# Performance work log

Hardware: AMD Instinct MI355X
Metric: run time of the kernel (lower is better)

Reference implementation:

```python
import jax, jax.numpy as jnp
import numpy as np

ALPHA = 32.0
RANK = 16
SCALE = ALPHA / RANK


def setup_inputs() -> dict:
    key = jax.random.key(0)
    k1, k2, k3, k4, k5 = jax.random.split(key, 5)
    B, S, D_IN, D_OUT, N = 4, 2048, 4096, 4096, 8
    x = jax.random.normal(k1, (B, S, D_IN), dtype=jnp.float32)
    routing_w = jax.random.uniform(k2, (B, N), dtype=jnp.float32)
    W_base = jax.random.normal(k3, (D_OUT, D_IN), dtype=jnp.float32) * 0.02
    lora_down = jax.random.normal(k4, (N, RANK, D_IN), dtype=jnp.float32) * 0.02
    lora_up = jax.random.normal(k5, (N, D_OUT, RANK), dtype=jnp.float32) * 0.02
    return {"x": x, "routing_w": routing_w, "W_base": W_base,
            "lora_down": lora_down, "lora_up": lora_up}


def reference(x, routing_w, W_base, lora_down, lora_up):
    # base linear: [B,S,D_in] @ [D_out,D_in]^T -> [B,S,D_out]
    base_out = jnp.einsum('bsi,oi->bso', x, W_base)
    # per-expert LoRA down-proj: [B,S,D_in] x [N,R,D_in] -> [B,N,S,R]
    down = jnp.einsum('bsi,nri->bnsr', x, lora_down)
    # up-proj + scale: [B,N,S,R] x [N,D_out,R] -> [B,N,S,D_out]
    up = jnp.einsum('bnsr,nor->bnso', down, lora_up) * SCALE
    # routing-weighted sum over experts: [B,N] x [B,N,S,D_out] -> [B,S,D_out]
    adapter_out = jnp.einsum('bn,bnso->bso', routing_w, up)
    return base_out + adapter_out
```

## Files before the change

kernel.cpp:

```cpp
#include <hip/hip_runtime.h>
#include <hip/hip_bf16.h>
#include <stdint.h>

#define TOK    8192
#define DIN    4096
#define DOUT   4096
#define NEXP   8
#define RK     16
#define NRANK  128
#define KE     4224
#define SEQB   2048
#define LSCALE 2.0f
#define KSPLIT 4
#define KSLICE (DIN / KSPLIT)

typedef __attribute__((ext_vector_type(8))) short bf8_t;
typedef __attribute__((ext_vector_type(4))) float f4_t;

__device__ __forceinline__ void async_copy16(const void* g, void* l) {
  __builtin_amdgcn_global_load_lds((const __attribute__((address_space(1))) void*)g,
                                   (__attribute__((address_space(3))) void*)l,
                                   16, 0, 0);
}

__device__ __forceinline__ ushort f2bf(float f) {
  __hip_bfloat16 h = __float2bfloat16(f);
  return *reinterpret_cast<ushort*>(&h);
}

#define R0 (TOK * DIN / 8)
#define R1 (DOUT * DIN / 8)
#define R2 (DOUT * NEXP * 2)
#define R3 (NRANK * DIN / 8)
#define RTOT (R0 + R1 + R2 + R3)

__global__ __launch_bounds__(256)
void cvt_all_kernel(const float* __restrict__ x, const float* __restrict__ wb,
                    const float* __restrict__ lu, const float* __restrict__ ld,
                    ushort* __restrict__ Xe, ushort* __restrict__ Wc,
                    ushort* __restrict__ Ldb) {
  int i = blockIdx.x * 256 + threadIdx.x;
  const float* src;
  ushort* dst;
  if (i < R0) {
    int t = i >> 9;
    int c = (i & 511) * 8;
    src = x + (size_t)t * DIN + c;
    dst = Xe + (size_t)t * KE + c;
  } else if (i < R0 + R1) {
    int j = i - R0;
    int t = j >> 9;
    int c = (j & 511) * 8;
    src = wb + (size_t)t * DIN + c;
    dst = Wc + (size_t)t * KE + c;
  } else if (i < R0 + R1 + R2) {
    int j = i - (R0 + R1);
    int o = j >> 4;
    int rem = j & 15;
    int n = rem >> 1;
    int half = rem & 1;
    src = lu + ((size_t)n * DOUT + o) * RK + half * 8;
    dst = Wc + (size_t)o * KE + DIN + n * RK + half * 8;
  } else {
    int j = i - (R0 + R1 + R2);
    src = ld + (size_t)j * 8;
    dst = Ldb + (size_t)j * 8;
  }
  const float4* s = reinterpret_cast<const float4*>(src);
  float4 a = s[0], b = s[1];
  union { ushort u[8]; uint4 v; } o;
  o.u[0]=f2bf(a.x); o.u[1]=f2bf(a.y); o.u[2]=f2bf(a.z); o.u[3]=f2bf(a.w);
  o.u[4]=f2bf(b.x); o.u[5]=f2bf(b.y); o.u[6]=f2bf(b.z); o.u[7]=f2bf(b.w);
  *reinterpret_cast<uint4*>(dst) = o.v;
}

template<int KLEN, int LDB, int MODE>
__global__ __launch_bounds__(256)
void gemm128(const ushort* __restrict__ A,
             const ushort* __restrict__ Bm,
             float* __restrict__ C) {
  __shared__ __align__(16) ushort As[128 * 32];
  __shared__ __align__(16) ushort Bs[128 * 32];

  const int tid  = threadIdx.x;
  const int wave = tid >> 6;
  const int lane = tid & 63;

  int bm, bn;
  if (MODE == 0) {
    int bid = blockIdx.x;
    int xcd = bid & 7;
    int idx = bid >> 3;
    int nt  = xcd * 4 + (idx & 3);
    int mt  = idx >> 2;
    bm = mt * 128;
    bn = nt * 128;
  } else {
    bm = blockIdx.y * 128;
    bn = blockIdx.x * 128;
  }
  const int wm = wave & 1, wn = wave >> 1;

  f4_t acc[4][4];
#pragma unroll
  for (int i = 0; i < 4; i++)
#pragma unroll
    for (int j = 0; j < 4; j++) acc[i][j] = (f4_t){0.f, 0.f, 0.f, 0.f};

  const int f0 = tid * 8;
  const int r0 = f0 >> 5, c0 = f0 & 31;
  const int f1 = (256 + tid) * 8;
  const int r1 = f1 >> 5, c1 = f1 & 31;
  const int l0 = (wave << 6) * 8;
  const int l1 = (256 + (wave << 6)) * 8;

  const ushort* Ar = As + (wm * 64 + (lane & 15)) * 32 + (lane >> 4) * 8;
  const ushort* Br = Bs + (wn * 64 + (lane & 15)) * 32 + (lane >> 4) * 8;

  const int kbase = (MODE == 1) ? blockIdx.z * KSLICE : 0;
  const int kend  = kbase + KLEN;

  for (int k0 = kbase; k0 < kend; k0 += 32) {
    __syncthreads();
    async_copy16(A  + (size_t)(bm + r0) * KE  + k0 + c0, (void*)(As + l0));
    async_copy16(A  + (size_t)(bm + r1) * KE  + k0 + c1, (void*)(As + l1));
    async_copy16(Bm + (size_t)(bn + r0) * LDB + k0 + c0, (void*)(Bs + l0));
    async_copy16(Bm + (size_t)(bn + r1) * LDB + k0 + c1, (void*)(Bs + l1));
    __syncthreads();
    bf8_t av[4], bv[4];
#pragma unroll
    for (int i = 0; i < 4; i++) av[i] = *(const bf8_t*)(Ar + i * 16 * 32);
#pragma unroll
    for (int j = 0; j < 4; j++) bv[j] = *(const bf8_t*)(Br + j * 16 * 32);
#pragma unroll
    for (int i = 0; i < 4; i++)
#pragma unroll
      for (int j = 0; j < 4; j++)
        acc[i][j] = __builtin_amdgcn_mfma_f32_16x16x32_bf16(av[i], bv[j], acc[i][j], 0, 0, 0);
  }

  if (MODE == 0) {
#pragma unroll
    for (int i = 0; i < 4; i++) {
      int row = bm + wm * 64 + i * 16 + (lane >> 4) * 4;
#pragma unroll
      for (int j = 0; j < 4; j++) {
        int col = bn + wn * 64 + j * 16 + (lane & 15);
#pragma unroll
        for (int rr = 0; rr < 4; rr++)
          C[(size_t)(row + rr) * DOUT + col] = acc[i][j][rr];
      }
    }
  } else {
    float* Dz = C + (size_t)blockIdx.z * TOK * NRANK;
#pragma unroll
    for (int i = 0; i < 4; i++) {
      int row = bm + wm * 64 + i * 16 + (lane >> 4) * 4;
#pragma unroll
      for (int j = 0; j < 4; j++) {
        int col = wn * 64 + j * 16 + (lane & 15);
#pragma unroll
        for (int rr = 0; rr < 4; rr++)
          Dz[(size_t)(row + rr) * NRANK + col] = acc[i][j][rr];
      }
    }
  }
}

__global__ void scale_store_kernel(const float* __restrict__ D32,
                                   const float* __restrict__ rw,
                                   ushort* __restrict__ Xe) {
  int i = blockIdx.x * 256 + threadIdx.x;
  int t = i >> 5;
  int g = (i & 31) * 4;
  size_t base = (size_t)t * NRANK + g;
  const size_t ss = (size_t)TOK * NRANK;
  float4 a = *reinterpret_cast<const float4*>(D32 + base);
  float4 b = *reinterpret_cast<const float4*>(D32 + ss + base);
  float4 c = *reinterpret_cast<const float4*>(D32 + 2 * ss + base);
  float4 d = *reinterpret_cast<const float4*>(D32 + 3 * ss + base);
  int n = g >> 4;
  int bb = t / SEQB;
  float s = rw[bb * NEXP + n] * LSCALE;
  union { ushort u[4]; uint2 v; } o;
  o.u[0] = f2bf((a.x + b.x + c.x + d.x) * s);
  o.u[1] = f2bf((a.y + b.y + c.y + d.y) * s);
  o.u[2] = f2bf((a.z + b.z + c.z + d.z) * s);
  o.u[3] = f2bf((a.w + b.w + c.w + d.w) * s);
  *reinterpret_cast<uint2*>(Xe + (size_t)t * KE + DIN + g) = o.v;
}

extern "C" void kernel_launch(void* const* d_in, const int* in_sizes, int n_in,
                              void* d_out, int out_size, void* d_ws, size_t ws_size,
                              hipStream_t stream) {
  const float* x  = (const float*)d_in[0];
  const float* rw = (const float*)d_in[1];
  const float* wb = (const float*)d_in[2];
  const float* ld = (const float*)d_in[3];
  const float* lu = (const float*)d_in[4];
  float* out = (float*)d_out;

  ushort* Xe  = (ushort*)d_ws;
  ushort* Wc  = Xe + (size_t)TOK * KE;
  ushort* Ldb = Wc + (size_t)DOUT * KE;
  float*  D32 = (float*)(Ldb + (size_t)NRANK * DIN);

  cvt_all_kernel<<<RTOT / 256, 256, 0, stream>>>(x, wb, lu, ld, Xe, Wc, Ldb);

  gemm128<KSLICE, DIN, 1><<<dim3(1, TOK / 128, KSPLIT), 256, 0, stream>>>(Xe, Ldb, D32);
  scale_store_kernel<<<TOK * NRANK / 4 / 256, 256, 0, stream>>>(D32, rw, Xe);
  gemm128<KE, KE, 0><<<dim3((TOK / 128) * (DOUT / 128)), 256, 0, stream>>>(Xe, Wc, out);
}
```

Baseline: 673.4 us.

## Use 256x256 double-buffered tiles for main fused GEMM

Splits the templated GEMM into a dedicated down-projection kernel and a new main GEMM. The main GEMM uses 256x256 output tiles with a 128x128 per-wave sub-tile and double-buffered LDS, prefetching the next K-step while the current one computes. The goal is to raise arithmetic intensity and hide global-load latency. The cost is 256 accumulator registers per thread at one block per CU, fewer blocks (512), and a different XCD tile mapping, so spills or low occupancy are possible.

```diff
diff --git a/kernel.cpp b/kernel.cpp
--- a/kernel.cpp
+++ b/kernel.cpp
@@ -74,31 +74,17 @@
   *reinterpret_cast<uint4*>(dst) = o.v;
 }
 
-template<int KLEN, int LDB, int MODE>
 __global__ __launch_bounds__(256)
-void gemm128(const ushort* __restrict__ A,
-             const ushort* __restrict__ Bm,
-             float* __restrict__ C) {
+void gemm_down(const ushort* __restrict__ A,
+               const ushort* __restrict__ Bm,
+               float* __restrict__ C) {
   __shared__ __align__(16) ushort As[128 * 32];
   __shared__ __align__(16) ushort Bs[128 * 32];
 
   const int tid  = threadIdx.x;
   const int wave = tid >> 6;
   const int lane = tid & 63;
-
-  int bm, bn;
-  if (MODE == 0) {
-    int bid = blockIdx.x;
-    int xcd = bid & 7;
-    int idx = bid >> 3;
-    int nt  = xcd * 4 + (idx & 3);
-    int mt  = idx >> 2;
-    bm = mt * 128;
-    bn = nt * 128;
-  } else {
-    bm = blockIdx.y * 128;
-    bn = blockIdx.x * 128;
-  }
+  const int bm = blockIdx.y * 128;
   const int wm = wave & 1, wn = wave >> 1;
 
   f4_t acc[4][4];
@@ -117,15 +103,15 @@
   const ushort* Ar = As + (wm * 64 + (lane & 15)) * 32 + (lane >> 4) * 8;
   const ushort* Br = Bs + (wn * 64 + (lane & 15)) * 32 + (lane >> 4) * 8;
 
-  const int kbase = (MODE == 1) ? blockIdx.z * KSLICE : 0;
-  const int kend  = kbase + KLEN;
+  const int kbase = blockIdx.z * KSLICE;
+  const int kend  = kbase + KSLICE;
 
   for (int k0 = kbase; k0 < kend; k0 += 32) {
     __syncthreads();
     async_copy16(A  + (size_t)(bm + r0) * KE  + k0 + c0, (void*)(As + l0));
     async_copy16(A  + (size_t)(bm + r1) * KE  + k0 + c1, (void*)(As + l1));
-    async_copy16(Bm + (size_t)(bn + r0) * LDB + k0 + c0, (void*)(Bs + l0));
-    async_copy16(Bm + (size_t)(bn + r1) * LDB + k0 + c1, (void*)(Bs + l1));
+    async_copy16(Bm + (size_t)r0 * DIN + k0 + c0, (void*)(Bs + l0));
+    async_copy16(Bm + (size_t)r1 * DIN + k0 + c1, (void*)(Bs + l1));
     __syncthreads();
     bf8_t av[4], bv[4];
 #pragma unroll
@@ -139,30 +125,103 @@
         acc[i][j] = __builtin_amdgcn_mfma_f32_16x16x32_bf16(av[i], bv[j], acc[i][j], 0, 0, 0);
   }
 
-  if (MODE == 0) {
-#pragma unroll
-    for (int i = 0; i < 4; i++) {
-      int row = bm + wm * 64 + i * 16 + (lane >> 4) * 4;
-#pragma unroll
-      for (int j = 0; j < 4; j++) {
-        int col = bn + wn * 64 + j * 16 + (lane & 15);
-#pragma unroll
-        for (int rr = 0; rr < 4; rr++)
-          C[(size_t)(row + rr) * DOUT + col] = acc[i][j][rr];
+  float* Dz = C + (size_t)blockIdx.z * TOK * NRANK;
+#pragma unroll
+  for (int i = 0; i < 4; i++) {
+    int row = bm + wm * 64 + i * 16 + (lane >> 4) * 4;
+#pragma unroll
+    for (int j = 0; j < 4; j++) {
+      int col = wn * 64 + j * 16 + (lane & 15);
+#pragma unroll
+      for (int rr = 0; rr < 4; rr++)
+        Dz[(size_t)(row + rr) * NRANK + col] = acc[i][j][rr];
+    }
+  }
+}
+
+#define NK (KE / 32)
+
+__global__ __launch_bounds__(256, 1)
+void gemm_main(const ushort* __restrict__ A,
+               const ushort* __restrict__ Bm,
+               float* __restrict__ C) {
+  __shared__ __align__(16) ushort As[2][256 * 32];
+  __shared__ __align__(16) ushort Bs[2][256 * 32];
+
+  const int tid  = threadIdx.x;
+  const int wave = tid >> 6;
+  const int lane = tid & 63;
+
+  const int bid = blockIdx.x;
+  const int xcd = bid & 7;
+  const int idx = bid >> 3;
+  const int nt  = xcd * 2 + (idx & 1);
+  const int mt  = idx >> 1;
+  const int bm = mt * 256;
+  const int bn = nt * 256;
+  const int wm = wave & 1, wn = wave >> 1;
+
+  f4_t acc[8][8];
+#pragma unroll
+  for (int i = 0; i < 8; i++)
+#pragma unroll
+    for (int j = 0; j < 8; j++) acc[i][j] = (f4_t){0.f, 0.f, 0.f, 0.f};
+
+  const int srow   = wave * 64 + (lane >> 2);
+  const int schunk = (lane & 3) * 8;
+  const ushort* gA = A  + (size_t)(bm + srow) * KE + schunk;
+  const ushort* gB = Bm + (size_t)(bn + srow) * KE + schunk;
+  const int lbase = wave * 64 * 32;
+
+  const int aoff = (wm * 128 + (lane & 15)) * 32 + (lane >> 4) * 8;
+  const int boff = (wn * 128 + (lane & 15)) * 32 + (lane >> 4) * 8;
+
+  {
+    const ushort* a = gA;
+    const ushort* b = gB;
+#pragma unroll
+    for (int j2 = 0; j2 < 4; j2++) {
+      async_copy16(a + (size_t)j2 * 16 * KE, (void*)(&As[0][lbase + j2 * 16 * 32]));
+      async_copy16(b + (size_t)j2 * 16 * KE, (void*)(&Bs[0][lbase + j2 * 16 * 32]));
+    }
+  }
+
+  for (int k = 0; k < NK; k++) {
+    const int buf = k & 1;
+    __syncthreads();
+    if (k + 1 < NK) {
+      const int nbuf = (k + 1) & 1;
+      const ushort* a = gA + (size_t)(k + 1) * 32;
+      const ushort* b = gB + (size_t)(k + 1) * 32;
+#pragma unroll
+      for (int j2 = 0; j2 < 4; j2++) {
+        async_copy16(a + (size_t)j2 * 16 * KE, (void*)(&As[nbuf][lbase + j2 * 16 * 32]));
+        async_copy16(b + (size_t)j2 * 16 * KE, (void*)(&Bs[nbuf][lbase + j2 * 16 * 32]));
       }
     }
-  } else {
-    float* Dz = C + (size_t)blockIdx.z * TOK * NRANK;
-#pragma unroll
-    for (int i = 0; i < 4; i++) {
-      int row = bm + wm * 64 + i * 16 + (lane >> 4) * 4;
-#pragma unroll
-      for (int j = 0; j < 4; j++) {
-        int col = wn * 64 + j * 16 + (lane & 15);
-#pragma unroll
-        for (int rr = 0; rr < 4; rr++)
-          Dz[(size_t)(row + rr) * NRANK + col] = acc[i][j][rr];
-      }
+    const ushort* Ar = &As[buf][aoff];
+    const ushort* Br = &Bs[buf][boff];
+    bf8_t bv[8];
+#pragma unroll
+    for (int jn = 0; jn < 8; jn++) bv[jn] = *(const bf8_t*)(Br + jn * 16 * 32);
+#pragma unroll
+    for (int i = 0; i < 8; i++) {
+      bf8_t av = *(const bf8_t*)(Ar + i * 16 * 32);
+#pragma unroll
+      for (int jn = 0; jn < 8; jn++)
+        acc[i][jn] = __builtin_amdgcn_mfma_f32_16x16x32_bf16(av, bv[jn], acc[i][jn], 0, 0, 0);
+    }
+  }
+
+#pragma unroll
+  for (int i = 0; i < 8; i++) {
+    int row = bm + wm * 128 + i * 16 + (lane >> 4) * 4;
+#pragma unroll
+    for (int jn = 0; jn < 8; jn++) {
+      int col = bn + wn * 128 + jn * 16 + (lane & 15);
+#pragma unroll
+      for (int rr = 0; rr < 4; rr++)
+        C[(size_t)(row + rr) * DOUT + col] = acc[i][jn][rr];
     }
   }
 }
@@ -207,7 +266,7 @@
 
   cvt_all_kernel<<<RTOT / 256, 256, 0, stream>>>(x, wb, lu, ld, Xe, Wc, Ldb);
 
-  gemm128<KSLICE, DIN, 1><<<dim3(1, TOK / 128, KSPLIT), 256, 0, stream>>>(Xe, Ldb, D32);
+  gemm_down<<<dim3(1, TOK / 128, KSPLIT), 256, 0, stream>>>(Xe, Ldb, D32);
   scale_store_kernel<<<TOK * NRANK / 4 / 256, 256, 0, stream>>>(D32, rw, Xe);
-  gemm128<KE, KE, 0><<<dim3((TOK / 128) * (DOUT / 128)), 256, 0, stream>>>(Xe, Wc, out);
-}
+  gemm_main<<<dim3((TOK / 256) * (DOUT / 256)), 256, 0, stream>>>(Xe, Wc, out);
+}
```

Result: slower. 750.0 us (+11.4%).
